# Kernel tuning notes

Measured on AMD Instinct MI355X. Metric: run time of the kernel, lower is better.

## Reference

```python
import jax, jax.numpy as jnp
import numpy as np

N = 50000
E = 800000
IN_DIM = 16
HID = 64
HEADS = 4
OUT_DIM = 2
LN_EPS = 1e-5
NEG_SLOPE = 0.2  # GATConv default negative_slope


def _layernorm(h, g, b):
    mu = jnp.mean(h, axis=-1, keepdims=True)
    var = jnp.var(h, axis=-1, keepdims=True)
    return (h - mu) * jax.lax.rsqrt(var + LN_EPS) * g + b


def _gat_layer(h, src, dst, w, a_src, a_dst, b):
    # PyG GATConv, concat=False: per-head channels C=HID, head-averaged output.
    n = h.shape[0]
    xp = (h @ w).reshape(n, HEADS, HID)          # [N,H,C]
    e_src = jnp.sum(xp * a_src, axis=-1)          # [N,H]
    e_dst = jnp.sum(xp * a_dst, axis=-1)          # [N,H]
    e = jax.nn.leaky_relu(e_src[src] + e_dst[dst], negative_slope=NEG_SLOPE)  # [Etot,H]
    # numerically-stable segment softmax over edges grouped by target node
    m = jax.lax.stop_gradient(jax.ops.segment_max(e, dst, num_segments=n))
    ex = jnp.exp(e - m[dst])
    denom = jax.ops.segment_sum(ex, dst, num_segments=n)
    alpha = ex / denom[dst]                       # [Etot,H]
    out = jax.ops.segment_sum(xp[src] * alpha[:, :, None], dst, num_segments=n)  # [N,H,C]
    return jnp.mean(out, axis=1) + b              # mean over heads (concat=False) + bias


def _forward(x, edge_index, w0, a_src0, a_dst0, b0, ln0_g, ln0_b,
             w1, a_src1, a_dst1, b1, ln1_g, ln1_b,
             gru_w_ih, gru_w_hh, gru_b_ih, gru_b_hh,
             d0_w, d0_b, d1_w, d1_b, d2_w, d2_b):
    n = x.shape[0]
    # add_self_loops=True
    loops = jnp.arange(n, dtype=edge_index.dtype)
    src = jnp.concatenate([edge_index[0], loops])
    dst = jnp.concatenate([edge_index[1], loops])
    # GAT layer 1 + LayerNorm + ReLU (dropout is identity in eval)
    h = _gat_layer(x, src, dst, w0, a_src0, a_dst0, b0)
    h = jax.nn.relu(_layernorm(h, ln0_g, ln0_b))
    # GAT layer 2 + LayerNorm (last layer -> no ReLU)
    h = _gat_layer(h, src, dst, w1, a_src1, a_dst1, b1)
    h = _layernorm(h, ln1_g, ln1_b)
    # single-timestep GRU with zero initial hidden state (PyTorch GRU cell math)
    h0 = jnp.zeros((n, HID), dtype=h.dtype)
    gi = h @ gru_w_ih.T + gru_b_ih
    gh = h0 @ gru_w_hh.T + gru_b_hh
    gi_r, gi_z, gi_n = jnp.split(gi, 3, axis=-1)
    gh_r, gh_z, gh_n = jnp.split(gh, 3, axis=-1)
    r = jax.nn.sigmoid(gi_r + gh_r)
    z = jax.nn.sigmoid(gi_z + gh_z)
    cand = jnp.tanh(gi_n + r * gh_n)
    temporal = (1.0 - z) * cand + z * h0
    # MLP decoder on cat([temporal_features, x])
    d = jnp.concatenate([temporal, x], axis=-1)
    d = jax.nn.relu(d @ d0_w + d0_b)
    d = jax.nn.relu(d @ d1_w + d1_b)
    d = d @ d2_w + d2_b
    return jnp.clip(d, -0.5, 0.5)


def setup_inputs():
    key = jax.random.key(0)
    ks = jax.random.split(key, 16)
    rn = lambda k, shape, s=0.05: jax.random.normal(k, shape, dtype=jnp.float32) * s
    return {
        'x': jax.random.normal(ks[0], (N, IN_DIM), dtype=jnp.float32),
        'edge_index': jax.random.randint(ks[1], (2, E), 0, N, dtype=jnp.int32),
        'w0': rn(ks[2], (IN_DIM, HEADS * HID)),
        'a_src0': rn(ks[3], (HEADS, HID)),
        'a_dst0': rn(ks[4], (HEADS, HID)),
        'b0': jnp.zeros((HID,), jnp.float32),
        'ln0_g': jnp.ones((HID,), jnp.float32),
        'ln0_b': jnp.zeros((HID,), jnp.float32),
        'w1': rn(ks[5], (HID, HEADS * HID)),
        'a_src1': rn(ks[6], (HEADS, HID)),
        'a_dst1': rn(ks[7], (HEADS, HID)),
        'b1': jnp.zeros((HID,), jnp.float32),
        'ln1_g': jnp.ones((HID,), jnp.float32),
        'ln1_b': jnp.zeros((HID,), jnp.float32),
        'gru_w_ih': rn(ks[8], (3 * HID, HID)),
        'gru_w_hh': rn(ks[9], (3 * HID, HID)),
        'gru_b_ih': jnp.zeros((3 * HID,), jnp.float32),
        'gru_b_hh': jnp.zeros((3 * HID,), jnp.float32),
        'd0_w': rn(ks[10], (HID + IN_DIM, HID)),
        'd0_b': jnp.zeros((HID,), jnp.float32),
        'd1_w': rn(ks[11], (HID, HID // 2)),
        'd1_b': jnp.zeros((HID // 2,), jnp.float32),
        'd2_w': rn(ks[12], (HID // 2, OUT_DIM)),
        'd2_b': jnp.zeros((OUT_DIM,), jnp.float32),
    }


def reference(x, edge_index, w0, a_src0, a_dst0, b0, ln0_g, ln0_b,
              w1, a_src1, a_dst1, b1, ln1_g, ln1_b,
              gru_w_ih, gru_w_hh, gru_b_ih, gru_b_hh,
              d0_w, d0_b, d1_w, d1_b, d2_w, d2_b):
    return _forward(x, edge_index, w0, a_src0, a_dst0, b0, ln0_g, ln0_b,
                    w1, a_src1, a_dst1, b1, ln1_g, ln1_b,
                    gru_w_ih, gru_w_hh, gru_b_ih, gru_b_hh,
                    d0_w, d0_b, d1_w, d1_b, d2_w, d2_b)
```

## Files before the change

kernel.cpp:

```cpp
#include <hip/hip_runtime.h>
#include <hip/hip_fp16.h>
#include <math.h>

#define NN 50000
#define NE 800000
#define ETOT (NE + NN)
#define HID 64
#define CH 256
#define IND 16
#define LN_EPS 1e-5f
#define NSLOPE 0.2f
#define ELLW 64
#define EB ((ETOT + 255) / 256)
#define PB ((NN + 31) / 32)

__device__ __forceinline__ float lrelu(float v){ return v > 0.f ? v : NSLOPE * v; }
__device__ __forceinline__ float sigf(float v){ return 1.f / (1.f + __expf(-v)); }


__global__ __launch_bounds__(256) void k_build_proj1(const int* __restrict__ ei,
    int* __restrict__ deg, unsigned short* __restrict__ colE,
    const float* __restrict__ h, const float* __restrict__ w,
    const float* __restrict__ asr, const float* __restrict__ adr,
    __half* __restrict__ xph, float* __restrict__ es, float* __restrict__ ed){
  __shared__ float w_s[IND * CH];
  __shared__ float h_s[IND][36];
  __shared__ float as_s[CH], ad_s[CH];
  const int t = threadIdx.x;

  if (blockIdx.x >= PB){
    const int bb = blockIdx.x - PB;
    const int part = bb & 7;
    const int e = (bb >> 3) * 256 + t;
    if (e < ETOT){
      int s, d;
      if (e < NE){ s = ei[e]; d = ei[NE + e]; } else { s = d = e - NE; }
      if ((d & 7) == part){
        const int slot = atomicAdd(&deg[d], 1);
        if (slot < ELLW) colE[d * ELLW + slot] = (unsigned short)s;
      }
    }
    return;
  }

  const int tile = blockIdx.x * 32;
  for (int i = t; i < IND * CH; i += 256) w_s[i] = w[i];
  as_s[t] = asr[t]; ad_s[t] = adr[t];
  for (int i = t; i < 32 * IND; i += 256){
    int n = i / IND, k = i % IND;
    int nn = tile + n;
    h_s[k][n] = (nn < NN) ? h[nn * IND + k] : 0.f;
  }
  __syncthreads();

  const int wv = t >> 6, l = t & 63;
  const int tc = l & 31, th = l >> 5;
  const int g = wv * 2 + th;
  const int c0 = tc * 4;
  const int hA = tc >> 4;

  float acc[4][8];
  #pragma unroll
  for (int j = 0; j < 4; ++j)
    #pragma unroll
    for (int i = 0; i < 8; ++i) acc[j][i] = 0.f;

  #pragma unroll 4
  for (int k = 0; k < IND; ++k){
    const float4 wa = *(const float4*)&w_s[k * CH + c0];
    const float4 wb = *(const float4*)&w_s[k * CH + c0 + 128];
    const float4 hv = *(const float4*)&h_s[k][g * 4];
    const float hj0 = hv.x, hj1 = hv.y, hj2 = hv.z, hj3 = hv.w;
    #define STEP(j, hjv) \
      acc[j][0] = fmaf(hjv, wa.x, acc[j][0]); \
      acc[j][1] = fmaf(hjv, wa.y, acc[j][1]); \
      acc[j][2] = fmaf(hjv, wa.z, acc[j][2]); \
      acc[j][3] = fmaf(hjv, wa.w, acc[j][3]); \
      acc[j][4] = fmaf(hjv, wb.x, acc[j][4]); \
      acc[j][5] = fmaf(hjv, wb.y, acc[j][5]); \
      acc[j][6] = fmaf(hjv, wb.z, acc[j][6]); \
      acc[j][7] = fmaf(hjv, wb.w, acc[j][7]);
    STEP(0, hj0) STEP(1, hj1) STEP(2, hj2) STEP(3, hj3)
    #undef STEP
  }

  #pragma unroll
  for (int j = 0; j < 4; ++j){
    const int nj = tile + g * 4 + j;
    float pa = 0.f, pb = 0.f, qa = 0.f, qb = 0.f;
    #pragma unroll
    for (int i = 0; i < 4; ++i){
      pa = fmaf(acc[j][i],     as_s[c0 + i],       pa);
      pb = fmaf(acc[j][4 + i], as_s[c0 + 128 + i], pb);
      qa = fmaf(acc[j][i],     ad_s[c0 + i],       qa);
      qb = fmaf(acc[j][4 + i], ad_s[c0 + 128 + i], qb);
    }
    #pragma unroll
    for (int d = 8; d; d >>= 1){
      pa += __shfl_xor(pa, d); pb += __shfl_xor(pb, d);
      qa += __shfl_xor(qa, d); qb += __shfl_xor(qb, d);
    }
    if (nj < NN){
      union { uint2 u; __half2 h2[2]; } oA, oB;
      oA.h2[0] = __float22half2_rn(make_float2(acc[j][0], acc[j][1]));
      oA.h2[1] = __float22half2_rn(make_float2(acc[j][2], acc[j][3]));
      oB.h2[0] = __float22half2_rn(make_float2(acc[j][4], acc[j][5]));
      oB.h2[1] = __float22half2_rn(make_float2(acc[j][6], acc[j][7]));
      *(uint2*)&xph[(size_t)nj * CH + c0]       = oA.u;
      *(uint2*)&xph[(size_t)nj * CH + c0 + 128] = oB.u;
      if ((tc & 15) == 0){
        es[nj * 4 + hA]     = pa;
        es[nj * 4 + hA + 2] = pb;
        ed[nj * 4 + hA]     = qa;
        ed[nj * 4 + hA + 2] = qb;
      }
    }
  }
}


template<int K, bool WHALF>
__global__ __launch_bounds__(256) void k_proj(const float* __restrict__ h,
    const float* __restrict__ w, const float* __restrict__ asr,
    const float* __restrict__ adr, __half* __restrict__ xph,
    float* __restrict__ es, float* __restrict__ ed){
  __shared__ float  w_sf[WHALF ? 1 : K * CH];
  __shared__ __half w_sh[WHALF ? K * CH : 1];
  __shared__ float h_s[K][36];
  __shared__ float as_s[CH], ad_s[CH];
  const int t = threadIdx.x;
  if (WHALF){
    for (int i = t; i < K * CH; i += 256) w_sh[i] = __float2half(w[i]);
  } else {
    for (int i = t; i < K * CH; i += 256) w_sf[i] = w[i];
  }
  as_s[t] = asr[t]; ad_s[t] = adr[t];
  const int wv = t >> 6, l = t & 63;
  const int tc = l & 31, th = l >> 5;
  const int g = wv * 2 + th;
  const int c0 = tc * 4;
  const int hA = tc >> 4;

  for (int tile = blockIdx.x * 32; tile < NN; tile += gridDim.x * 32){
    __syncthreads();
    for (int i = t; i < 32 * K; i += 256){
      int n = i / K, k = i % K;
      int nn = tile + n;
      h_s[k][n] = (nn < NN) ? h[nn * K + k] : 0.f;
    }
    __syncthreads();

    float acc[4][8];
    #pragma unroll
    for (int j = 0; j < 4; ++j)
      #pragma unroll
      for (int i = 0; i < 8; ++i) acc[j][i] = 0.f;

    #pragma unroll 4
    for (int k = 0; k < K; ++k){
      float4 wa, wb;
      if (WHALF){
        union { uint2 u; __half2 h2[2]; } A, B;
        A.u = *(const uint2*)&w_sh[k * CH + c0];
        B.u = *(const uint2*)&w_sh[k * CH + c0 + 128];
        const float2 a01 = __half22float2(A.h2[0]), a23 = __half22float2(A.h2[1]);
        const float2 b01 = __half22float2(B.h2[0]), b23 = __half22float2(B.h2[1]);
        wa.x = a01.x; wa.y = a01.y; wa.z = a23.x; wa.w = a23.y;
        wb.x = b01.x; wb.y = b01.y; wb.z = b23.x; wb.w = b23.y;
      } else {
        wa = *(const float4*)&w_sf[k * CH + c0];
        wb = *(const float4*)&w_sf[k * CH + c0 + 128];
      }
      const float4 hv = *(const float4*)&h_s[k][g * 4];
      const float hj0 = hv.x, hj1 = hv.y, hj2 = hv.z, hj3 = hv.w;
      #define STEP(j, hjv) \
        acc[j][0] = fmaf(hjv, wa.x, acc[j][0]); \
        acc[j][1] = fmaf(hjv, wa.y, acc[j][1]); \
        acc[j][2] = fmaf(hjv, wa.z, acc[j][2]); \
        acc[j][3] = fmaf(hjv, wa.w, acc[j][3]); \
        acc[j][4] = fmaf(hjv, wb.x, acc[j][4]); \
        acc[j][5] = fmaf(hjv, wb.y, acc[j][5]); \
        acc[j][6] = fmaf(hjv, wb.z, acc[j][6]); \
        acc[j][7] = fmaf(hjv, wb.w, acc[j][7]);
      STEP(0, hj0) STEP(1, hj1) STEP(2, hj2) STEP(3, hj3)
      #undef STEP
    }

    #pragma unroll
    for (int j = 0; j < 4; ++j){
      const int nj = tile + g * 4 + j;
      float pa = 0.f, pb = 0.f, qa = 0.f, qb = 0.f;
      #pragma unroll
      for (int i = 0; i < 4; ++i){
        pa = fmaf(acc[j][i],     as_s[c0 + i],       pa);
        pb = fmaf(acc[j][4 + i], as_s[c0 + 128 + i], pb);
        qa = fmaf(acc[j][i],     ad_s[c0 + i],       qa);
        qb = fmaf(acc[j][4 + i], ad_s[c0 + 128 + i], qb);
      }
      #pragma unroll
      for (int d = 8; d; d >>= 1){
        pa += __shfl_xor(pa, d); pb += __shfl_xor(pb, d);
        qa += __shfl_xor(qa, d); qb += __shfl_xor(qb, d);
      }
      if (nj < NN){
        union { uint2 u; __half2 h2[2]; } oA, oB;
        oA.h2[0] = __float22half2_rn(make_float2(acc[j][0], acc[j][1]));
        oA.h2[1] = __float22half2_rn(make_float2(acc[j][2], acc[j][3]));
        oB.h2[0] = __float22half2_rn(make_float2(acc[j][4], acc[j][5]));
        oB.h2[1] = __float22half2_rn(make_float2(acc[j][6], acc[j][7]));
        *(uint2*)&xph[(size_t)nj * CH + c0]       = oA.u;
        *(uint2*)&xph[(size_t)nj * CH + c0 + 128] = oB.u;
        if ((tc & 15) == 0){
          es[nj * 4 + hA]     = pa;
          es[nj * 4 + hA + 2] = pb;
          ed[nj * 4 + hA]     = qa;
          ed[nj * 4 + hA + 2] = qb;
        }
      }
    }
  }
}


template<int DO_RELU>
__global__ __launch_bounds__(256) void k_agg(const __half* __restrict__ xph,
    const float4* __restrict__ es4, const float4* __restrict__ ed4,
    const int* __restrict__ deg, const unsigned short* __restrict__ colE,
    const float* __restrict__ bias, const float* __restrict__ lng,
    const float* __restrict__ lnb, float* __restrict__ hout){
  __shared__ float pbuf[4][2][32][4];
  const int wid = threadIdx.x >> 6, lane = threadIdx.x & 63;
  const int half = lane >> 5, l32 = lane & 31;
  const int n = blockIdx.x * 8 + wid * 2 + half;
  const int head = l32 >> 3;
  const int c8 = l32 * 8;
  const int dg = deg[n];
  const int dmax = max(dg, __shfl(dg, lane ^ 32));
  const float4 edn = ed4[n];
  float den = 0.f;
  float acc[8];
  #pragma unroll
  for (int i = 0; i < 8; ++i) acc[i] = 0.f;

  for (int base = 0; base < dmax; base += 32){
    const int cmax = min(dmax - base, 32);
    const int myS = (int)colE[n * ELLW + min(base + l32, dg - 1)];
    const float4 e = es4[myS];
    const bool act = (base + l32 < dg);
    float4 p4;
    p4.x = act ? __expf(lrelu(e.x + edn.x)) : 0.f;
    p4.y = act ? __expf(lrelu(e.y + edn.y)) : 0.f;
    p4.z = act ? __expf(lrelu(e.z + edn.z)) : 0.f;
    p4.w = act ? __expf(lrelu(e.w + edn.w)) : 0.f;
    *(float4*)&pbuf[wid][half][l32][0] = p4;
    const int sOff = myS * CH;

    for (int u0 = 0; u0 < cmax; u0 += 8){
      float pw[8]; uint4 xv[8];
      #pragma unroll
      for (int u = 0; u < 8; ++u){
        const int uu = u0 + u, us = uu & 31;
        const int so = __shfl(sOff, (lane & 32) + us);
        xv[u] = *(const uint4*)&xph[so + c8];
        pw[u] = (uu < cmax) ? pbuf[wid][half][us][head] : 0.f;
      }
      #pragma unroll
      for (int u = 0; u < 8; ++u){
        union { uint4 q; __half2 h2[4]; } cv; cv.q = xv[u];
        const float2 f0 = __half22float2(cv.h2[0]);
        const float2 f1 = __half22float2(cv.h2[1]);
        const float2 f2 = __half22float2(cv.h2[2]);
        const float2 f3 = __half22float2(cv.h2[3]);
        den += pw[u];
        acc[0] = fmaf(f0.x, pw[u], acc[0]); acc[1] = fmaf(f0.y, pw[u], acc[1]);
        acc[2] = fmaf(f1.x, pw[u], acc[2]); acc[3] = fmaf(f1.y, pw[u], acc[3]);
        acc[4] = fmaf(f2.x, pw[u], acc[4]); acc[5] = fmaf(f2.y, pw[u], acc[5]);
        acc[6] = fmaf(f3.x, pw[u], acc[6]); acc[7] = fmaf(f3.y, pw[u], acc[7]);
      }
    }
  }

  const float inv = 1.f / den;
  #pragma unroll
  for (int i = 0; i < 8; ++i) acc[i] *= inv;
  #pragma unroll
  for (int i = 0; i < 8; ++i){
    acc[i] += __shfl_xor(acc[i], 8);
    acc[i] += __shfl_xor(acc[i], 16);
  }
  const int ch0 = (l32 & 7) * 8;
  const float4 bA = *(const float4*)&bias[ch0];
  const float4 bB = *(const float4*)&bias[ch0 + 4];
  acc[0] = acc[0]*0.25f + bA.x; acc[1] = acc[1]*0.25f + bA.y;
  acc[2] = acc[2]*0.25f + bA.z; acc[3] = acc[3]*0.25f + bA.w;
  acc[4] = acc[4]*0.25f + bB.x; acc[5] = acc[5]*0.25f + bB.y;
  acc[6] = acc[6]*0.25f + bB.z; acc[7] = acc[7]*0.25f + bB.w;
  float s = 0.f, q = 0.f;
  #pragma unroll
  for (int i = 0; i < 8; ++i){ s += acc[i]; q += acc[i]*acc[i]; }
  #pragma unroll
  for (int d = 4; d; d >>= 1){ s += __shfl_xor(s, d); q += __shfl_xor(q, d); }
  const float mu = s * (1.f / 64.f);
  const float var = q * (1.f / 64.f) - mu * mu;
  const float rs = rsqrtf(var + LN_EPS);
  const float4 gA = *(const float4*)&lng[ch0];
  const float4 gB = *(const float4*)&lng[ch0 + 4];
  const float4 tA = *(const float4*)&lnb[ch0];
  const float4 tB = *(const float4*)&lnb[ch0 + 4];
  acc[0] = (acc[0]-mu)*rs*gA.x + tA.x; acc[1] = (acc[1]-mu)*rs*gA.y + tA.y;
  acc[2] = (acc[2]-mu)*rs*gA.z + tA.z; acc[3] = (acc[3]-mu)*rs*gA.w + tA.w;
  acc[4] = (acc[4]-mu)*rs*gB.x + tB.x; acc[5] = (acc[5]-mu)*rs*gB.y + tB.y;
  acc[6] = (acc[6]-mu)*rs*gB.z + tB.z; acc[7] = (acc[7]-mu)*rs*gB.w + tB.w;
  if (DO_RELU){
    #pragma unroll
    for (int i = 0; i < 8; ++i) acc[i] = fmaxf(acc[i], 0.f);
  }
  if (l32 < 8){
    float4 oA, oB;
    oA.x = acc[0]; oA.y = acc[1]; oA.z = acc[2]; oA.w = acc[3];
    oB.x = acc[4]; oB.y = acc[5]; oB.z = acc[6]; oB.w = acc[7];
    *(float4*)&hout[n * HID + l32 * 8]     = oA;
    *(float4*)&hout[n * HID + l32 * 8 + 4] = oB;
  }
}


#define WTS 196

__global__ __launch_bounds__(256) void k_gru(const float* __restrict__ h,
    const float* __restrict__ wih, const float* __restrict__ bih,
    const float* __restrict__ bhh, float* __restrict__ tmp){
  __shared__ __half wT[64 * WTS];
  __shared__ float h_s[64][34];
  __shared__ float bi_s[192], bh_s[192];
  const int t = threadIdx.x;
  for (int i = t; i < 192 * 64; i += 256)
    wT[(i & 63) * WTS + (i >> 6)] = __float2half(wih[i]);
  if (t < 192){ bi_s[t] = bih[t]; bh_s[t] = bhh[t]; }
  const int col = t & 15, gg = t >> 4;
  const int c0 = col * 4;

  for (int tile = blockIdx.x * 32; tile < NN; tile += gridDim.x * 32){
    __syncthreads();
    for (int i = t; i < 32 * 64; i += 256){
      int nidx = i >> 6, k = i & 63;
      int nn = tile + nidx;
      h_s[k][nidx] = (nn < NN) ? h[nn * 64 + k] : 0.f;
    }
    __syncthreads();

    float ar[2][4] = {{0}}, az[2][4] = {{0}}, an[2][4] = {{0}};
    #pragma unroll 4
    for (int k = 0; k < 64; ++k){
      union { uint2 u; __half2 h2[2]; } R, Z, N_;
      R.u  = *(const uint2*)&wT[k * WTS + c0];
      Z.u  = *(const uint2*)&wT[k * WTS + 64 + c0];
      N_.u = *(const uint2*)&wT[k * WTS + 128 + c0];
      const float2 r01 = __half22float2(R.h2[0]),  r23 = __half22float2(R.h2[1]);
      const float2 z01 = __half22float2(Z.h2[0]),  z23 = __half22float2(Z.h2[1]);
      const float2 n01 = __half22float2(N_.h2[0]), n23 = __half22float2(N_.h2[1]);
      const float h0v = h_s[k][gg * 2];
      const float h1v = h_s[k][gg * 2 + 1];
      ar[0][0] = fmaf(h0v, r01.x, ar[0][0]); ar[0][1] = fmaf(h0v, r01.y, ar[0][1]);
      ar[0][2] = fmaf(h0v, r23.x, ar[0][2]); ar[0][3] = fmaf(h0v, r23.y, ar[0][3]);
      az[0][0] = fmaf(h0v, z01.x, az[0][0]); az[0][1] = fmaf(h0v, z01.y, az[0][1]);
      az[0][2] = fmaf(h0v, z23.x, az[0][2]); az[0][3] = fmaf(h0v, z23.y, az[0][3]);
      an[0][0] = fmaf(h0v, n01.x, an[0][0]); an[0][1] = fmaf(h0v, n01.y, an[0][1]);
      an[0][2] = fmaf(h0v, n23.x, an[0][2]); an[0][3] = fmaf(h0v, n23.y, an[0][3]);
      ar[1][0] = fmaf(h1v, r01.x, ar[1][0]); ar[1][1] = fmaf(h1v, r01.y, ar[1][1]);
      ar[1][2] = fmaf(h1v, r23.x, ar[1][2]); ar[1][3] = fmaf(h1v, r23.y, ar[1][3]);
      az[1][0] = fmaf(h1v, z01.x, az[1][0]); az[1][1] = fmaf(h1v, z01.y, az[1][1]);
      az[1][2] = fmaf(h1v, z23.x, az[1][2]); az[1][3] = fmaf(h1v, z23.y, az[1][3]);
      an[1][0] = fmaf(h1v, n01.x, an[1][0]); an[1][1] = fmaf(h1v, n01.y, an[1][1]);
      an[1][2] = fmaf(h1v, n23.x, an[1][2]); an[1][3] = fmaf(h1v, n23.y, an[1][3]);
    }

    #pragma unroll
    for (int j = 0; j < 2; ++j){
      const int nj = tile + gg * 2 + j;
      if (nj < NN){
        float tv[4];
        #pragma unroll
        for (int i = 0; i < 4; ++i){
          const int c = c0 + i;
          const float r  = sigf(ar[j][i] + bi_s[c] + bh_s[c]);
          const float zz = sigf(az[j][i] + bi_s[64 + c] + bh_s[64 + c]);
          const float cd = tanhf(an[j][i] + bi_s[128 + c] + r * bh_s[128 + c]);
          tv[i] = (1.f - zz) * cd;
        }
        float4 o; o.x = tv[0]; o.y = tv[1]; o.z = tv[2]; o.w = tv[3];
        *(float4*)&tmp[(size_t)nj * 64 + c0] = o;
      }
    }
  }
}


__global__ __launch_bounds__(256) void k_dec(const float* __restrict__ tmp,
    const float* __restrict__ x, const float* __restrict__ d0w,
    const float* __restrict__ d0b, const float* __restrict__ d1w,
    const float* __restrict__ d1b, const float* __restrict__ d2w,
    const float* __restrict__ d2b, float* __restrict__ out){
  __shared__ __half w0s[80 * 64];
  __shared__ __half w1s[64 * 32];
  __shared__ float w2s[64];
  __shared__ float b0s[64], b1s[32], b2s[2];
  __shared__ float dc[80][34];
  __shared__ float t0s[64][34];
  __shared__ float t1s[32][34];
  const int t = threadIdx.x;
  for (int i = t; i < 80 * 64; i += 256) w0s[i] = __float2half(d0w[i]);
  for (int i = t; i < 64 * 32; i += 256) w1s[i] = __float2half(d1w[i]);
  if (t < 64) w2s[t] = d2w[t];
  if (t < 64) b0s[t] = d0b[t];
  if (t < 32) b1s[t] = d1b[t];
  if (t < 2)  b2s[t] = d2b[t];

  for (int tile = blockIdx.x * 32; tile < NN; tile += gridDim.x * 32){
    __syncthreads();
    for (int i = t; i < 32 * 64; i += 256){
      int nidx = i >> 6, k = i & 63;
      int nn = tile + nidx;
      dc[k][nidx] = (nn < NN) ? tmp[(size_t)nn * 64 + k] : 0.f;
    }
    for (int i = t; i < 32 * 16; i += 256){
      int nidx = i >> 4, k = i & 15;
      int nn = tile + nidx;
      dc[64 + k][nidx] = (nn < NN) ? x[nn * IND + k] : 0.f;
    }
    __syncthreads();

    {
      const int col = t & 15, gg = t >> 4, c0 = col * 4;
      float a[2][4] = {{0}};
      #pragma unroll 4
      for (int k = 0; k < 80; ++k){
        union { uint2 u; __half2 h2[2]; } W;
        W.u = *(const uint2*)&w0s[k * 64 + c0];
        const float2 w01 = __half22float2(W.h2[0]), w23 = __half22float2(W.h2[1]);
        const float b0v = dc[k][gg * 2];
        const float b1v = dc[k][gg * 2 + 1];
        a[0][0] = fmaf(b0v, w01.x, a[0][0]); a[0][1] = fmaf(b0v, w01.y, a[0][1]);
        a[0][2] = fmaf(b0v, w23.x, a[0][2]); a[0][3] = fmaf(b0v, w23.y, a[0][3]);
        a[1][0] = fmaf(b1v, w01.x, a[1][0]); a[1][1] = fmaf(b1v, w01.y, a[1][1]);
        a[1][2] = fmaf(b1v, w23.x, a[1][2]); a[1][3] = fmaf(b1v, w23.y, a[1][3]);
      }
      #pragma unroll
      for (int j = 0; j < 2; ++j)
        #pragma unroll
        for (int i = 0; i < 4; ++i)
          t0s[c0 + i][gg * 2 + j] = fmaxf(a[j][i] + b0s[c0 + i], 0.f);
    }
    __syncthreads();

    {
      const int c1 = (t & 7) * 4, g1 = t >> 3;
      float a[4] = {0, 0, 0, 0};
      #pragma unroll 4
      for (int k = 0; k < 64; ++k){
        union { uint2 u; __half2 h2[2]; } W;
        W.u = *(const uint2*)&w1s[k * 32 + c1];
        const float2 w01 = __half22float2(W.h2[0]), w23 = __half22float2(W.h2[1]);
        const float bv = t0s[k][g1];
        a[0] = fmaf(bv, w01.x, a[0]); a[1] = fmaf(bv, w01.y, a[1]);
        a[2] = fmaf(bv, w23.x, a[2]); a[3] = fmaf(bv, w23.y, a[3]);
      }
      #pragma unroll
      for (int i = 0; i < 4; ++i)
        t1s[c1 + i][g1] = fmaxf(a[i] + b1s[c1 + i], 0.f);
    }
    __syncthreads();

    if (t < 64){
      const int nidx = t >> 1, o = t & 1;
      float a = b2s[o];
      #pragma unroll
      for (int k = 0; k < 32; ++k) a = fmaf(t1s[k][nidx], w2s[k * 2 + o], a);
      const int nn = tile + nidx;
      if (nn < NN) out[nn * 2 + o] = fminf(fmaxf(a, -0.5f), 0.5f);
    }
  }
}


extern "C" void kernel_launch(void* const* d_in, const int* in_sizes, int n_in,
                              void* d_out, int out_size, void* d_ws, size_t ws_size,
                              hipStream_t stream){
  (void)in_sizes; (void)n_in; (void)out_size; (void)ws_size;
  const float* x      = (const float*)d_in[0];
  const int*   ei     = (const int*)d_in[1];
  const float* w0     = (const float*)d_in[2];
  const float* as0    = (const float*)d_in[3];
  const float* ad0    = (const float*)d_in[4];
  const float* b0     = (const float*)d_in[5];
  const float* ln0g   = (const float*)d_in[6];
  const float* ln0b   = (const float*)d_in[7];
  const float* w1     = (const float*)d_in[8];
  const float* as1    = (const float*)d_in[9];
  const float* ad1    = (const float*)d_in[10];
  const float* b1     = (const float*)d_in[11];
  const float* ln1g   = (const float*)d_in[12];
  const float* ln1b   = (const float*)d_in[13];
  const float* wih    = (const float*)d_in[14];
  const float* bih    = (const float*)d_in[16];
  const float* bhh    = (const float*)d_in[17];
  const float* d0w    = (const float*)d_in[18];
  const float* d0b    = (const float*)d_in[19];
  const float* d1w    = (const float*)d_in[20];
  const float* d1b    = (const float*)d_in[21];
  const float* d2w    = (const float*)d_in[22];
  const float* d2b    = (const float*)d_in[23];
  float* outp = (float*)d_out;

  char* ws = (char*)d_ws;
  size_t o = 0;
  auto alloc = [&](size_t bytes) -> char* {
    char* r = ws + o;
    o += (bytes + 255) & ~(size_t)255;
    return r;
  };
  int*            deg  = (int*)           alloc(NN * sizeof(int));
  unsigned short* colE = (unsigned short*)alloc((size_t)NN * ELLW * sizeof(unsigned short));
  float*          es   = (float*)         alloc((size_t)NN * 4 * sizeof(float));
  float*          ed   = (float*)         alloc((size_t)NN * 4 * sizeof(float));
  __half*         xph  = (__half*)        alloc((size_t)NN * CH * sizeof(__half));
  float*          hbuf = (float*)         alloc((size_t)NN * HID * sizeof(float));
  float*          tmp  = (float*)         alloc((size_t)NN * HID * sizeof(float));

  hipMemsetAsync(deg, 0, NN * sizeof(int), stream);
  k_build_proj1<<<PB + 8 * EB, 256, 0, stream>>>(ei, deg, colE, x, w0, as0, ad0,
                                                 xph, es, ed);
  k_agg<1><<<NN / 8, 256, 0, stream>>>(xph, (const float4*)es, (const float4*)ed,
                                       deg, colE, b0, ln0g, ln0b, hbuf);
  k_proj<HID, true><<<(NN + 31) / 32, 256, 0, stream>>>(hbuf, w1, as1, ad1,
                                                        xph, es, ed);
  k_agg<0><<<NN / 8, 256, 0, stream>>>(xph, (const float4*)es, (const float4*)ed,
                                       deg, colE, b1, ln1g, ln1b, hbuf);
  k_gru<<<(NN + 31) / 32, 256, 0, stream>>>(hbuf, wih, bih, bhh, tmp);
  k_dec<<<(NN + 31) / 32, 256, 0, stream>>>(tmp, x, d0w, d0b, d1w, d1b, d2w, d2b,
                                            outp);
}
```

Baseline: 287.9 us.

## Use channel-group-major projection layout and thread-per-node aggregation with LayerNorm moved downstream

The projected features are stored in a channel-group-major layout: 8 groups of 8 channels, with the 4 heads interleaved. Aggregation changes from a wave per two nodes with shared-memory weights to one thread per (node, channel group). Each thread walks its node's neighbor list serially and writes a partial 8-channel output. LayerNorm (and ReLU) now runs in the next projection kernel and in the GRU kernel instead of inside aggregation. The aim is to replace per-wave shuffles and shared-memory traffic with simple per-thread gathers. In exchange, each thread does serial work proportional to node degree, es values are re-read 8 times, and the projection writes become scattered 2-byte half stores.

```diff
diff --git a/kernel.cpp b/kernel.cpp
--- a/kernel.cpp
+++ b/kernel.cpp
@@ -13,16 +13,18 @@
 #define ELLW 64
 #define EB ((ETOT + 255) / 256)
 #define PB ((NN + 31) / 32)
+#define AGB (((NN + 255) / 256) * 8)
 
 __device__ __forceinline__ float lrelu(float v){ return v > 0.f ? v : NSLOPE * v; }
 __device__ __forceinline__ float sigf(float v){ return 1.f / (1.f + __expf(-v)); }
+
 
 
 __global__ __launch_bounds__(256) void k_build_proj1(const int* __restrict__ ei,
     int* __restrict__ deg, unsigned short* __restrict__ colE,
     const float* __restrict__ h, const float* __restrict__ w,
     const float* __restrict__ asr, const float* __restrict__ adr,
-    __half* __restrict__ xph, float* __restrict__ es, float* __restrict__ ed){
+    __half* __restrict__ xphP, float* __restrict__ es, float* __restrict__ ed){
   __shared__ float w_s[IND * CH];
   __shared__ float h_s[IND][36];
   __shared__ float as_s[CH], ad_s[CH];
@@ -33,9 +35,9 @@
     const int part = bb & 7;
     const int e = (bb >> 3) * 256 + t;
     if (e < ETOT){
-      int s, d;
-      if (e < NE){ s = ei[e]; d = ei[NE + e]; } else { s = d = e - NE; }
+      const int d = (e < NE) ? ei[NE + e] : (e - NE);
       if ((d & 7) == part){
+        const int s = (e < NE) ? ei[e] : d;
         const int slot = atomicAdd(&deg[d], 1);
         if (slot < ELLW) colE[d * ELLW + slot] = (unsigned short)s;
       }
@@ -84,6 +86,9 @@
     #undef STEP
   }
 
+  const int oc = c0 & 63;
+  const int gI = oc >> 3;
+  const int cp = oc & 7;
   #pragma unroll
   for (int j = 0; j < 4; ++j){
     const int nj = tile + g * 4 + j;
@@ -101,13 +106,12 @@
       qa += __shfl_xor(qa, d); qb += __shfl_xor(qb, d);
     }
     if (nj < NN){
-      union { uint2 u; __half2 h2[2]; } oA, oB;
-      oA.h2[0] = __float22half2_rn(make_float2(acc[j][0], acc[j][1]));
-      oA.h2[1] = __float22half2_rn(make_float2(acc[j][2], acc[j][3]));
-      oB.h2[0] = __float22half2_rn(make_float2(acc[j][4], acc[j][5]));
-      oB.h2[1] = __float22half2_rn(make_float2(acc[j][6], acc[j][7]));
-      *(uint2*)&xph[(size_t)nj * CH + c0]       = oA.u;
-      *(uint2*)&xph[(size_t)nj * CH + c0 + 128] = oB.u;
+      __half* wbase = &xphP[(((size_t)gI * NN + nj) * 8 + cp) * 4];
+      #pragma unroll
+      for (int i = 0; i < 4; ++i){
+        wbase[i * 4 + hA]     = __float2half(acc[j][i]);
+        wbase[i * 4 + hA + 2] = __float2half(acc[j][4 + i]);
+      }
       if ((tc & 15) == 0){
         es[nj * 4 + hA]     = pa;
         es[nj * 4 + hA + 2] = pb;
@@ -119,224 +123,194 @@
 }
 
 
-template<int K, bool WHALF>
-__global__ __launch_bounds__(256) void k_proj(const float* __restrict__ h,
+__global__ __launch_bounds__(256) void k_proj2(const float* __restrict__ hP,
     const float* __restrict__ w, const float* __restrict__ asr,
-    const float* __restrict__ adr, __half* __restrict__ xph,
+    const float* __restrict__ adr, const float* __restrict__ lng,
+    const float* __restrict__ lnb, __half* __restrict__ xphP,
     float* __restrict__ es, float* __restrict__ ed){
-  __shared__ float  w_sf[WHALF ? 1 : K * CH];
-  __shared__ __half w_sh[WHALF ? K * CH : 1];
-  __shared__ float h_s[K][36];
+  __shared__ __half w_sh[HID * CH];
+  __shared__ float h_s[HID][36];
   __shared__ float as_s[CH], ad_s[CH];
+  __shared__ float lg_s[64], lb_s[64], mu_s[32], rs_s[32];
   const int t = threadIdx.x;
-  if (WHALF){
-    for (int i = t; i < K * CH; i += 256) w_sh[i] = __float2half(w[i]);
-  } else {
-    for (int i = t; i < K * CH; i += 256) w_sf[i] = w[i];
-  }
+  for (int i = t; i < HID * CH; i += 256) w_sh[i] = __float2half(w[i]);
   as_s[t] = asr[t]; ad_s[t] = adr[t];
+  if (t < 64){ lg_s[t] = lng[t]; lb_s[t] = lnb[t]; }
+
+  const int tile = blockIdx.x * 32;
+  for (int i = t; i < 32 * HID; i += 256){
+    int n = i >> 6, k = i & 63;
+    int nn = tile + n;
+    h_s[k][n] = (nn < NN) ? hP[((size_t)(k >> 3) * NN + nn) * 8 + (k & 7)] : 0.f;
+  }
+  __syncthreads();
+  if (t < 32){
+    float s = 0.f, q = 0.f;
+    for (int k = 0; k < 64; ++k){ const float v = h_s[k][t]; s += v; q += v * v; }
+    const float mu = s * (1.f / 64.f);
+    mu_s[t] = mu;
+    rs_s[t] = rsqrtf(q * (1.f / 64.f) - mu * mu + LN_EPS);
+  }
+  __syncthreads();
+  for (int i = t; i < 32 * 64; i += 256){
+    const int k = i >> 5, n = i & 31;
+    float v = (h_s[k][n] - mu_s[n]) * rs_s[n] * lg_s[k] + lb_s[k];
+    h_s[k][n] = fmaxf(v, 0.f);
+  }
+  __syncthreads();
+
   const int wv = t >> 6, l = t & 63;
   const int tc = l & 31, th = l >> 5;
   const int g = wv * 2 + th;
   const int c0 = tc * 4;
   const int hA = tc >> 4;
 
-  for (int tile = blockIdx.x * 32; tile < NN; tile += gridDim.x * 32){
-    __syncthreads();
-    for (int i = t; i < 32 * K; i += 256){
-      int n = i / K, k = i % K;
-      int nn = tile + n;
-      h_s[k][n] = (nn < NN) ? h[nn * K + k] : 0.f;
-    }
-    __syncthreads();
-
-    float acc[4][8];
-    #pragma unroll
-    for (int j = 0; j < 4; ++j)
-      #pragma unroll
-      for (int i = 0; i < 8; ++i) acc[j][i] = 0.f;
-
-    #pragma unroll 4
-    for (int k = 0; k < K; ++k){
-      float4 wa, wb;
-      if (WHALF){
-        union { uint2 u; __half2 h2[2]; } A, B;
-        A.u = *(const uint2*)&w_sh[k * CH + c0];
-        B.u = *(const uint2*)&w_sh[k * CH + c0 + 128];
-        const float2 a01 = __half22float2(A.h2[0]), a23 = __half22float2(A.h2[1]);
-        const float2 b01 = __half22float2(B.h2[0]), b23 = __half22float2(B.h2[1]);
-        wa.x = a01.x; wa.y = a01.y; wa.z = a23.x; wa.w = a23.y;
-        wb.x = b01.x; wb.y = b01.y; wb.z = b23.x; wb.w = b23.y;
-      } else {
-        wa = *(const float4*)&w_sf[k * CH + c0];
-        wb = *(const float4*)&w_sf[k * CH + c0 + 128];
-      }
-      const float4 hv = *(const float4*)&h_s[k][g * 4];
-      const float hj0 = hv.x, hj1 = hv.y, hj2 = hv.z, hj3 = hv.w;
-      #define STEP(j, hjv) \
-        acc[j][0] = fmaf(hjv, wa.x, acc[j][0]); \
-        acc[j][1] = fmaf(hjv, wa.y, acc[j][1]); \
-        acc[j][2] = fmaf(hjv, wa.z, acc[j][2]); \
-        acc[j][3] = fmaf(hjv, wa.w, acc[j][3]); \
-        acc[j][4] = fmaf(hjv, wb.x, acc[j][4]); \
-        acc[j][5] = fmaf(hjv, wb.y, acc[j][5]); \
-        acc[j][6] = fmaf(hjv, wb.z, acc[j][6]); \
-        acc[j][7] = fmaf(hjv, wb.w, acc[j][7]);
-      STEP(0, hj0) STEP(1, hj1) STEP(2, hj2) STEP(3, hj3)
-      #undef STEP
-    }
-
-    #pragma unroll
-    for (int j = 0; j < 4; ++j){
-      const int nj = tile + g * 4 + j;
-      float pa = 0.f, pb = 0.f, qa = 0.f, qb = 0.f;
+  float acc[4][8];
+  #pragma unroll
+  for (int j = 0; j < 4; ++j)
+    #pragma unroll
+    for (int i = 0; i < 8; ++i) acc[j][i] = 0.f;
+
+  #pragma unroll 4
+  for (int k = 0; k < HID; ++k){
+    union { uint2 u; __half2 h2[2]; } A, B;
+    A.u = *(const uint2*)&w_sh[k * CH + c0];
+    B.u = *(const uint2*)&w_sh[k * CH + c0 + 128];
+    const float2 a01 = __half22float2(A.h2[0]), a23 = __half22float2(A.h2[1]);
+    const float2 b01 = __half22float2(B.h2[0]), b23 = __half22float2(B.h2[1]);
+    float4 wa, wb;
+    wa.x = a01.x; wa.y = a01.y; wa.z = a23.x; wa.w = a23.y;
+    wb.x = b01.x; wb.y = b01.y; wb.z = b23.x; wb.w = b23.y;
+    const float4 hv = *(const float4*)&h_s[k][g * 4];
+    const float hj0 = hv.x, hj1 = hv.y, hj2 = hv.z, hj3 = hv.w;
+    #define STEP(j, hjv) \
+      acc[j][0] = fmaf(hjv, wa.x, acc[j][0]); \
+      acc[j][1] = fmaf(hjv, wa.y, acc[j][1]); \
+      acc[j][2] = fmaf(hjv, wa.z, acc[j][2]); \
+      acc[j][3] = fmaf(hjv, wa.w, acc[j][3]); \
+      acc[j][4] = fmaf(hjv, wb.x, acc[j][4]); \
+      acc[j][5] = fmaf(hjv, wb.y, acc[j][5]); \
+      acc[j][6] = fmaf(hjv, wb.z, acc[j][6]); \
+      acc[j][7] = fmaf(hjv, wb.w, acc[j][7]);
+    STEP(0, hj0) STEP(1, hj1) STEP(2, hj2) STEP(3, hj3)
+    #undef STEP
+  }
+
+  const int oc = c0 & 63;
+  const int gI = oc >> 3;
+  const int cp = oc & 7;
+  #pragma unroll
+  for (int j = 0; j < 4; ++j){
+    const int nj = tile + g * 4 + j;
+    float pa = 0.f, pb = 0.f, qa = 0.f, qb = 0.f;
+    #pragma unroll
+    for (int i = 0; i < 4; ++i){
+      pa = fmaf(acc[j][i],     as_s[c0 + i],       pa);
+      pb = fmaf(acc[j][4 + i], as_s[c0 + 128 + i], pb);
+      qa = fmaf(acc[j][i],     ad_s[c0 + i],       qa);
+      qb = fmaf(acc[j][4 + i], ad_s[c0 + 128 + i], qb);
+    }
+    #pragma unroll
+    for (int d = 8; d; d >>= 1){
+      pa += __shfl_xor(pa, d); pb += __shfl_xor(pb, d);
+      qa += __shfl_xor(qa, d); qb += __shfl_xor(qb, d);
+    }
+    if (nj < NN){
+      __half* wbase = &xphP[(((size_t)gI * NN + nj) * 8 + cp) * 4];
       #pragma unroll
       for (int i = 0; i < 4; ++i){
-        pa = fmaf(acc[j][i],     as_s[c0 + i],       pa);
-        pb = fmaf(acc[j][4 + i], as_s[c0 + 128 + i], pb);
-        qa = fmaf(acc[j][i],     ad_s[c0 + i],       qa);
-        qb = fmaf(acc[j][4 + i], ad_s[c0 + 128 + i], qb);
-      }
-      #pragma unroll
-      for (int d = 8; d; d >>= 1){
-        pa += __shfl_xor(pa, d); pb += __shfl_xor(pb, d);
-        qa += __shfl_xor(qa, d); qb += __shfl_xor(qb, d);
-      }
-      if (nj < NN){
-        union { uint2 u; __half2 h2[2]; } oA, oB;
-        oA.h2[0] = __float22half2_rn(make_float2(acc[j][0], acc[j][1]));
-        oA.h2[1] = __float22half2_rn(make_float2(acc[j][2], acc[j][3]));
-        oB.h2[0] = __float22half2_rn(make_float2(acc[j][4], acc[j][5]));
-        oB.h2[1] = __float22half2_rn(make_float2(acc[j][6], acc[j][7]));
-        *(uint2*)&xph[(size_t)nj * CH + c0]       = oA.u;
-        *(uint2*)&xph[(size_t)nj * CH + c0 + 128] = oB.u;
-        if ((tc & 15) == 0){
-          es[nj * 4 + hA]     = pa;
-          es[nj * 4 + hA + 2] = pb;
-          ed[nj * 4 + hA]     = qa;
-          ed[nj * 4 + hA + 2] = qb;
-        }
+        wbase[i * 4 + hA]     = __float2half(acc[j][i]);
+        wbase[i * 4 + hA + 2] = __float2half(acc[j][4 + i]);
+      }
+      if ((tc & 15) == 0){
+        es[nj * 4 + hA]     = pa;
+        es[nj * 4 + hA + 2] = pb;
+        ed[nj * 4 + hA]     = qa;
+        ed[nj * 4 + hA + 2] = qb;
       }
     }
   }
 }
 
 
-template<int DO_RELU>
-__global__ __launch_bounds__(256) void k_agg(const __half* __restrict__ xph,
+__global__ __launch_bounds__(256) void k_agg(const __half* __restrict__ xphP,
     const float4* __restrict__ es4, const float4* __restrict__ ed4,
     const int* __restrict__ deg, const unsigned short* __restrict__ colE,
-    const float* __restrict__ bias, const float* __restrict__ lng,
-    const float* __restrict__ lnb, float* __restrict__ hout){
-  __shared__ float pbuf[4][2][32][4];
-  const int wid = threadIdx.x >> 6, lane = threadIdx.x & 63;
-  const int half = lane >> 5, l32 = lane & 31;
-  const int n = blockIdx.x * 8 + wid * 2 + half;
-  const int head = l32 >> 3;
-  const int c8 = l32 * 8;
-  const int dg = deg[n];
-  const int dmax = max(dg, __shfl(dg, lane ^ 32));
+    const float* __restrict__ bias, float* __restrict__ houtP){
+  const int g = blockIdx.x & 7;
+  const int n = (blockIdx.x >> 3) * 256 + threadIdx.x;
+  if (n >= NN) return;
+  const int dg = min(deg[n], ELLW);
   const float4 edn = ed4[n];
-  float den = 0.f;
-  float acc[8];
+  const __half* __restrict__ xb = xphP + (size_t)g * NN * 32;
+  float acc[4][8];
   #pragma unroll
-  for (int i = 0; i < 8; ++i) acc[i] = 0.f;
-
-  for (int base = 0; base < dmax; base += 32){
-    const int cmax = min(dmax - base, 32);
-    const int myS = (int)colE[n * ELLW + min(base + l32, dg - 1)];
-    const float4 e = es4[myS];
-    const bool act = (base + l32 < dg);
-    float4 p4;
-    p4.x = act ? __expf(lrelu(e.x + edn.x)) : 0.f;
-    p4.y = act ? __expf(lrelu(e.y + edn.y)) : 0.f;
-    p4.z = act ? __expf(lrelu(e.z + edn.z)) : 0.f;
-    p4.w = act ? __expf(lrelu(e.w + edn.w)) : 0.f;
-    *(float4*)&pbuf[wid][half][l32][0] = p4;
-    const int sOff = myS * CH;
-
-    for (int u0 = 0; u0 < cmax; u0 += 8){
-      float pw[8]; uint4 xv[8];
-      #pragma unroll
-      for (int u = 0; u < 8; ++u){
-        const int uu = u0 + u, us = uu & 31;
-        const int so = __shfl(sOff, (lane & 32) + us);
-        xv[u] = *(const uint4*)&xph[so + c8];
-        pw[u] = (uu < cmax) ? pbuf[wid][half][us][head] : 0.f;
-      }
-      #pragma unroll
-      for (int u = 0; u < 8; ++u){
-        union { uint4 q; __half2 h2[4]; } cv; cv.q = xv[u];
-        const float2 f0 = __half22float2(cv.h2[0]);
-        const float2 f1 = __half22float2(cv.h2[1]);
-        const float2 f2 = __half22float2(cv.h2[2]);
-        const float2 f3 = __half22float2(cv.h2[3]);
-        den += pw[u];
-        acc[0] = fmaf(f0.x, pw[u], acc[0]); acc[1] = fmaf(f0.y, pw[u], acc[1]);
-        acc[2] = fmaf(f1.x, pw[u], acc[2]); acc[3] = fmaf(f1.y, pw[u], acc[3]);
-        acc[4] = fmaf(f2.x, pw[u], acc[4]); acc[5] = fmaf(f2.y, pw[u], acc[5]);
-        acc[6] = fmaf(f3.x, pw[u], acc[6]); acc[7] = fmaf(f3.y, pw[u], acc[7]);
-      }
-    }
-  }
-
-  const float inv = 1.f / den;
+  for (int h = 0; h < 4; ++h)
+    #pragma unroll
+    for (int c = 0; c < 8; ++c) acc[h][c] = 0.f;
+  float den0 = 0.f, den1 = 0.f, den2 = 0.f, den3 = 0.f;
+
+  int s = (int)colE[n * ELLW];
+  for (int j = 0; j < dg; ++j){
+    const int snext = (j + 1 < dg) ? (int)colE[n * ELLW + j + 1] : 0;
+    const float4 e = es4[s];
+    const uint4* xq = (const uint4*)&xb[(size_t)s * 32];
+    const uint4 q0 = xq[0], q1 = xq[1], q2 = xq[2], q3 = xq[3];
+    const float p0 = __expf(lrelu(e.x + edn.x));
+    const float p1 = __expf(lrelu(e.y + edn.y));
+    const float p2 = __expf(lrelu(e.z + edn.z));
+    const float p3 = __expf(lrelu(e.w + edn.w));
+    den0 += p0; den1 += p1; den2 += p2; den3 += p3;
+    #define ACCQ(q, cb) { \
+      union { uint4 u; __half2 hh[4]; } U; U.u = q; \
+      const float2 f01 = __half22float2(U.hh[0]); \
+      const float2 f23 = __half22float2(U.hh[1]); \
+      const float2 g01 = __half22float2(U.hh[2]); \
+      const float2 g23 = __half22float2(U.hh[3]); \
+      acc[0][cb]     = fmaf(p0, f01.x, acc[0][cb]); \
+      acc[1][cb]     = fmaf(p1, f01.y, acc[1][cb]); \
+      acc[2][cb]     = fmaf(p2, f23.x, acc[2][cb]); \
+      acc[3][cb]     = fmaf(p3, f23.y, acc[3][cb]); \
+      acc[0][cb + 1] = fmaf(p0, g01.x, acc[0][cb + 1]); \
+      acc[1][cb + 1] = fmaf(p1, g01.y, acc[1][cb + 1]); \
+      acc[2][cb + 1] = fmaf(p2, g23.x, acc[2][cb + 1]); \
+      acc[3][cb + 1] = fmaf(p3, g23.y, acc[3][cb + 1]); }
+    ACCQ(q0, 0) ACCQ(q1, 2) ACCQ(q2, 4) ACCQ(q3, 6)
+    #undef ACCQ
+    s = snext;
+  }
+
+  const float i0 = 1.f / den0, i1 = 1.f / den1, i2 = 1.f / den2, i3 = 1.f / den3;
+  const float4 bA = *(const float4*)&bias[g * 8];
+  const float4 bB = *(const float4*)&bias[g * 8 + 4];
+  float o[8];
   #pragma unroll
-  for (int i = 0; i < 8; ++i) acc[i] *= inv;
-  #pragma unroll
-  for (int i = 0; i < 8; ++i){
-    acc[i] += __shfl_xor(acc[i], 8);
-    acc[i] += __shfl_xor(acc[i], 16);
-  }
-  const int ch0 = (l32 & 7) * 8;
-  const float4 bA = *(const float4*)&bias[ch0];
-  const float4 bB = *(const float4*)&bias[ch0 + 4];
-  acc[0] = acc[0]*0.25f + bA.x; acc[1] = acc[1]*0.25f + bA.y;
-  acc[2] = acc[2]*0.25f + bA.z; acc[3] = acc[3]*0.25f + bA.w;
-  acc[4] = acc[4]*0.25f + bB.x; acc[5] = acc[5]*0.25f + bB.y;
-  acc[6] = acc[6]*0.25f + bB.z; acc[7] = acc[7]*0.25f + bB.w;
-  float s = 0.f, q = 0.f;
-  #pragma unroll
-  for (int i = 0; i < 8; ++i){ s += acc[i]; q += acc[i]*acc[i]; }
-  #pragma unroll
-  for (int d = 4; d; d >>= 1){ s += __shfl_xor(s, d); q += __shfl_xor(q, d); }
-  const float mu = s * (1.f / 64.f);
-  const float var = q * (1.f / 64.f) - mu * mu;
-  const float rs = rsqrtf(var + LN_EPS);
-  const float4 gA = *(const float4*)&lng[ch0];
-  const float4 gB = *(const float4*)&lng[ch0 + 4];
-  const float4 tA = *(const float4*)&lnb[ch0];
-  const float4 tB = *(const float4*)&lnb[ch0 + 4];
-  acc[0] = (acc[0]-mu)*rs*gA.x + tA.x; acc[1] = (acc[1]-mu)*rs*gA.y + tA.y;
-  acc[2] = (acc[2]-mu)*rs*gA.z + tA.z; acc[3] = (acc[3]-mu)*rs*gA.w + tA.w;
-  acc[4] = (acc[4]-mu)*rs*gB.x + tB.x; acc[5] = (acc[5]-mu)*rs*gB.y + tB.y;
-  acc[6] = (acc[6]-mu)*rs*gB.z + tB.z; acc[7] = (acc[7]-mu)*rs*gB.w + tB.w;
-  if (DO_RELU){
-    #pragma unroll
-    for (int i = 0; i < 8; ++i) acc[i] = fmaxf(acc[i], 0.f);
-  }
-  if (l32 < 8){
-    float4 oA, oB;
-    oA.x = acc[0]; oA.y = acc[1]; oA.z = acc[2]; oA.w = acc[3];
-    oB.x = acc[4]; oB.y = acc[5]; oB.z = acc[6]; oB.w = acc[7];
-    *(float4*)&hout[n * HID + l32 * 8]     = oA;
-    *(float4*)&hout[n * HID + l32 * 8 + 4] = oB;
-  }
+  for (int c = 0; c < 8; ++c)
+    o[c] = 0.25f * (acc[0][c] * i0 + acc[1][c] * i1 + acc[2][c] * i2 + acc[3][c] * i3);
+  float4 oA, oB;
+  oA.x = o[0] + bA.x; oA.y = o[1] + bA.y; oA.z = o[2] + bA.z; oA.w = o[3] + bA.w;
+  oB.x = o[4] + bB.x; oB.y = o[5] + bB.y; oB.z = o[6] + bB.z; oB.w = o[7] + bB.w;
+  float* op = houtP + ((size_t)g * NN + n) * 8;
+  *(float4*)op       = oA;
+  *(float4*)(op + 4) = oB;
 }
 
 
 #define WTS 196
 
-__global__ __launch_bounds__(256) void k_gru(const float* __restrict__ h,
+__global__ __launch_bounds__(256) void k_gru(const float* __restrict__ hP,
+    const float* __restrict__ lng, const float* __restrict__ lnb,
     const float* __restrict__ wih, const float* __restrict__ bih,
     const float* __restrict__ bhh, float* __restrict__ tmp){
   __shared__ __half wT[64 * WTS];
   __shared__ float h_s[64][34];
   __shared__ float bi_s[192], bh_s[192];
+  __shared__ float lg_s[64], lb_s[64], mu_s[32], rs_s[32];
   const int t = threadIdx.x;
   for (int i = t; i < 192 * 64; i += 256)
     wT[(i & 63) * WTS + (i >> 6)] = __float2half(wih[i]);
   if (t < 192){ bi_s[t] = bih[t]; bh_s[t] = bhh[t]; }
+  if (t < 64){ lg_s[t] = lng[t]; lb_s[t] = lnb[t]; }
   const int col = t & 15, gg = t >> 4;
   const int c0 = col * 4;
 
@@ -345,7 +319,20 @@
     for (int i = t; i < 32 * 64; i += 256){
       int nidx = i >> 6, k = i & 63;
       int nn = tile + nidx;
-      h_s[k][nidx] = (nn < NN) ? h[nn * 64 + k] : 0.f;
+      h_s[k][nidx] = (nn < NN) ? hP[((size_t)(k >> 3) * NN + nn) * 8 + (k & 7)] : 0.f;
+    }
+    __syncthreads();
+    if (t < 32){
+      float s = 0.f, q = 0.f;
+      for (int k = 0; k < 64; ++k){ const float v = h_s[k][t]; s += v; q += v * v; }
+      const float mu = s * (1.f / 64.f);
+      mu_s[t] = mu;
+      rs_s[t] = rsqrtf(q * (1.f / 64.f) - mu * mu + LN_EPS);
+    }
+    __syncthreads();
+    for (int i = t; i < 32 * 64; i += 256){
+      const int k = i >> 5, n = i & 31;
+      h_s[k][n] = (h_s[k][n] - mu_s[n]) * rs_s[n] * lg_s[k] + lb_s[k];
     }
     __syncthreads();
 
@@ -519,24 +506,23 @@
     o += (bytes + 255) & ~(size_t)255;
     return r;
   };
-  int*            deg  = (int*)           alloc(NN * sizeof(int));
-  unsigned short* colE = (unsigned short*)alloc((size_t)NN * ELLW * sizeof(unsigned short));
-  float*          es   = (float*)         alloc((size_t)NN * 4 * sizeof(float));
-  float*          ed   = (float*)         alloc((size_t)NN * 4 * sizeof(float));
-  __half*         xph  = (__half*)        alloc((size_t)NN * CH * sizeof(__half));
-  float*          hbuf = (float*)         alloc((size_t)NN * HID * sizeof(float));
-  float*          tmp  = (float*)         alloc((size_t)NN * HID * sizeof(float));
+  int*            deg   = (int*)           alloc(NN * sizeof(int));
+  unsigned short* colE  = (unsigned short*)alloc((size_t)NN * ELLW * sizeof(unsigned short));
+  float*          es    = (float*)         alloc((size_t)NN * 4 * sizeof(float));
+  float*          ed    = (float*)         alloc((size_t)NN * 4 * sizeof(float));
+  __half*         xphP  = (__half*)        alloc((size_t)NN * CH * sizeof(__half));
+  float*          hbufP = (float*)         alloc((size_t)NN * HID * sizeof(float));
+  float*          tmp   = (float*)         alloc((size_t)NN * HID * sizeof(float));
 
   hipMemsetAsync(deg, 0, NN * sizeof(int), stream);
   k_build_proj1<<<PB + 8 * EB, 256, 0, stream>>>(ei, deg, colE, x, w0, as0, ad0,
-                                                 xph, es, ed);
-  k_agg<1><<<NN / 8, 256, 0, stream>>>(xph, (const float4*)es, (const float4*)ed,
-                                       deg, colE, b0, ln0g, ln0b, hbuf);
-  k_proj<HID, true><<<(NN + 31) / 32, 256, 0, stream>>>(hbuf, w1, as1, ad1,
-                                                        xph, es, ed);
-  k_agg<0><<<NN / 8, 256, 0, stream>>>(xph, (const float4*)es, (const float4*)ed,
-                                       deg, colE, b1, ln1g, ln1b, hbuf);
-  k_gru<<<(NN + 31) / 32, 256, 0, stream>>>(hbuf, wih, bih, bhh, tmp);
+                                                 xphP, es, ed);
+  k_agg<<<AGB, 256, 0, stream>>>(xphP, (const float4*)es, (const float4*)ed,
+                                 deg, colE, b0, hbufP);
+  k_proj2<<<PB, 256, 0, stream>>>(hbufP, w1, as1, ad1, ln0g, ln0b, xphP, es, ed);
+  k_agg<<<AGB, 256, 0, stream>>>(xphP, (const float4*)es, (const float4*)ed,
+                                 deg, colE, b1, hbufP);
+  k_gru<<<(NN + 31) / 32, 256, 0, stream>>>(hbufP, ln1g, ln1b, wih, bih, bhh, tmp);
   k_dec<<<(NN + 31) / 32, 256, 0, stream>>>(tmp, x, d0w, d0b, d1w, d1b, d2w, d2b,
                                             outp);
 }
```

Measured after the change: 614.0 us. 113% more time.
